# Kernel optimization log

Measured on AMD Instinct MI355X. Metric: run time of the kernel, lower is better.

## Reference

```python
import jax, jax.numpy as jnp
import numpy as np

TAU = 0.1
B = 4        # number of batches
S = 256      # spatial extent per axis
K = 128      # max peaks per batch (original caps total at num_batches*128)
NEG = -jnp.inf


def _l2norm(x, eps=1e-12):
    n = jnp.sqrt(jnp.sum(x * x, axis=1, keepdims=True))
    return x / jnp.maximum(n, eps)


def _peak_pool(coords, feats, conf, mask):
    # Submanifold 3x3x3 sparse max-pool on conf and avg-pool on feats,
    # restricted to voxels with conf > tau (the original builds the spconv
    # tensors only from masked voxels). Neighbor lookup via sorted key hash.
    N = coords.shape[0]
    bidx = coords[:, 0]
    x, y, z = coords[:, 1], coords[:, 2], coords[:, 3]
    key = ((bidx * S + x) * S + y) * S + z
    order = jnp.argsort(key)
    skey = key[order]
    hmax = jnp.full((N,), NEG, dtype=conf.dtype)
    fsum = jnp.zeros_like(feats)
    cnt = jnp.zeros((N,), dtype=feats.dtype)
    for dx in (-1, 0, 1):
        for dy in (-1, 0, 1):
            for dz in (-1, 0, 1):
                nx, ny, nz = x + dx, y + dy, z + dz
                valid = (nx >= 0) & (nx < S) & (ny >= 0) & (ny < S) & (nz >= 0) & (nz < S)
                nkey = ((bidx * S + nx) * S + ny) * S + nz
                pos = jnp.minimum(jnp.searchsorted(skey, nkey), N - 1)
                j = order[pos]
                hit = valid & (skey[pos] == nkey) & mask[j]
                hmax = jnp.maximum(hmax, jnp.where(hit, conf[j], NEG))
                fsum = fsum + jnp.where(hit[:, None], feats[j], 0.0)
                cnt = cnt + hit.astype(feats.dtype)
    favg = fsum / jnp.maximum(cnt, 1.0)[:, None]
    return hmax, favg


def setup_inputs() -> dict:
    key = jax.random.key(0)
    ks = jax.random.split(key, 6)
    N, L, D = 800000, 64, 32
    batch = jax.random.randint(ks[0], (N, 1), 0, B, dtype=jnp.int32)
    xyz = jax.random.randint(ks[1], (N, 3), 0, S, dtype=jnp.int32)
    coords = jnp.concatenate([batch, xyz], axis=1)
    voxel_feats = jax.random.normal(ks[2], (N, L), jnp.float32)
    centroid_scores = jax.random.uniform(ks[3], (N, 1), jnp.float32)
    W = jax.random.normal(ks[4], (L, D), jnp.float32) * 0.05
    b = jnp.zeros((D,), jnp.float32)
    background = jax.random.normal(ks[5], (D,), jnp.float32) * 0.02
    return {"coords": coords, "voxel_feats": voxel_feats,
            "centroid_scores": centroid_scores, "W": W, "b": b,
            "background": background}


def reference(coords, voxel_feats, centroid_scores, W, b, background):
    conf = centroid_scores[:, 0]
    mask = conf > TAU
    hmax, peak_feats = _peak_pool(coords, voxel_feats, conf, mask)
    # CenterNet-style NMS: a masked voxel is a peak if it equals its local max
    peak_mask = mask & (hmax == conf)
    voxel_desc = _l2norm(voxel_feats @ W + b)           # [N, D]
    bidx = coords[:, 0]
    peak_conf, blocks = [], []
    for bi in range(B):
        score = jnp.where(peak_mask & (bidx == bi), conf, NEG)
        vals, idx = jax.lax.top_k(score, K)             # fixed K peaks/batch
        valid = jnp.isfinite(vals)
        cdesc = _l2norm(peak_feats[idx] @ W + b)        # [K, D]
        cdesc = jnp.where(valid[:, None], cdesc, 0.0)
        # per-batch layout: background descriptor first, then centroids
        blocks.append(jnp.concatenate([background[None, :], cdesc], axis=0))
        peak_conf.append(jnp.where(valid, vals, 0.0))
    full_desc = jnp.concatenate(blocks, axis=0)         # [B*(K+1), D]
    return jnp.stack(peak_conf, axis=0), voxel_desc, full_desc
```

## Files before the change

kernel.cpp:

```cpp
#include <hip/hip_runtime.h>
#include <math.h>

#define S 256
#define NB 4
#define TAU 0.1f
#define KSEL 128
#define LOG_TAB 21
#define TAB_SZ (1u << LOG_TAB)
#define TAB_MASK (TAB_SZ - 1)
#define EMPTY64 0xFFFFFFFFFFFFFFFFull
#define BM_WORDS (1u << 21)
#define NBINS 8192
#define BIN_BASE 0x3D800
#define CAND_CAP 4096
#define CPAD 32

typedef unsigned long long u64;
typedef unsigned int u32;

__device__ __forceinline__ u32 hash_key(int key) {
    u32 h = (u32)key * 0x9E3779B1u;
    h ^= h >> 15;
    return h & TAB_MASK;
}

__device__ __forceinline__ int conf_bin(float conf) {
    int bin = (int)(__float_as_uint(conf) >> 12) - BIN_BASE;
    return bin < 0 ? 0 : (bin > NBINS - 1 ? NBINS - 1 : bin);
}

__device__ __forceinline__ int tab_lookup(const u64* __restrict__ tab, int key) {
    u32 slot = hash_key(key);
    for (;;) {
        u64 e = tab[slot];
        if ((u32)(e >> 32) == (u32)key) return (int)(u32)e;
        if (e == EMPTY64) return -1;
        slot = (slot + 1) & TAB_MASK;
    }
}

__device__ __forceinline__ void desc_row(const float* __restrict__ feats,
                                         const float* __restrict__ W,
                                         const float* __restrict__ bias,
                                         float* __restrict__ voxel_desc, int i, int N) {
    if (i >= N) return;
    const float4* row4 = (const float4*)(feats + (size_t)i * 64);
    float4 r[16];
    #pragma unroll
    for (int k = 0; k < 16; k++) r[k] = row4[k];
    asm volatile("" ::: "memory");
    float acc[32];
    #pragma unroll
    for (int d = 0; d < 32; d++) acc[d] = bias[d];
    #pragma unroll
    for (int k = 0; k < 16; k++) {
        float4 f = r[k];
        const float* Wb = W + k * 4 * 32;
        #pragma unroll
        for (int d = 0; d < 32; d++) {
            acc[d] = fmaf(f.x, Wb[d], acc[d]);
            acc[d] = fmaf(f.y, Wb[32 + d], acc[d]);
            acc[d] = fmaf(f.z, Wb[64 + d], acc[d]);
            acc[d] = fmaf(f.w, Wb[96 + d], acc[d]);
        }
    }
    float ss = 0.f;
    #pragma unroll
    for (int d = 0; d < 32; d++) ss += acc[d] * acc[d];
    float inv = 1.0f / fmaxf(sqrtf(ss), 1e-12f);
    float4* out4 = (float4*)(voxel_desc + (size_t)i * 32);
    #pragma unroll
    for (int q = 0; q < 8; q++) {
        float4 o;
        o.x = acc[q * 4 + 0] * inv; o.y = acc[q * 4 + 1] * inv;
        o.z = acc[q * 4 + 2] * inv; o.w = acc[q * 4 + 3] * inv;
        out4[q] = o;
    }
}

__device__ __forceinline__ void insert_pt(const int* __restrict__ coords,
                                          const float* __restrict__ scores,
                                          u64* __restrict__ tab, u32* __restrict__ bm,
                                          int i, int N) {
    if (i >= N) return;
    int4 c = ((const int4*)coords)[i];
    float conf = scores[i];
    int key = ((c.x * S + c.y) * S + c.z) * S + c.w;
    if (conf > TAU) atomicOr(&bm[(u32)key >> 5], 1u << (key & 31));
    u64 ins = ((u64)(u32)key << 32) | (u32)i;
    u32 slot = hash_key(key);
    for (;;) {
        u64 e = tab[slot];
        if ((u32)(e >> 32) == (u32)key) { atomicMin(&tab[slot], ins); return; }
        if (e == EMPTY64) {
            u64 prev = atomicCAS(&tab[slot], EMPTY64, ins);
            if (prev == EMPTY64) return;
            if ((u32)(prev >> 32) == (u32)key) { atomicMin(&tab[slot], ins); return; }
        }
        slot = (slot + 1) & TAB_MASK;
    }
}

__global__ __launch_bounds__(256, 4) void k_ins_desc(const int* __restrict__ coords,
        const float* __restrict__ scores, u64* __restrict__ tab, u32* __restrict__ bm,
        const float* __restrict__ feats, const float* __restrict__ W,
        const float* __restrict__ bias, float* __restrict__ voxel_desc,
        int N, int nIns, int nDesc, int descRow0) {
    int g = blockIdx.x / 3, r = blockIdx.x % 3;
    if (r < 2) {
        int ib = g * 2 + r;
        if (ib >= nIns) return;
        insert_pt(coords, scores, tab, bm, ib * 256 + threadIdx.x, N);
    } else {
        if (g >= nDesc) return;
        desc_row(feats, W, bias, voxel_desc, descRow0 + g * 256 + threadIdx.x, N);
    }
}

__device__ __forceinline__ void peak_block(const int* __restrict__ coords,
        const float* __restrict__ scores, const u64* __restrict__ tab,
        const u32* __restrict__ bm, u64* __restrict__ peaks, int* __restrict__ cnt,
        int* __restrict__ hist, int N, int pcap, int pb) {
    int i = pb * 256 + threadIdx.x;
    bool alive = (i < N);
    int ii = alive ? i : 0;
    int4 c = ((const int4*)coords)[ii];
    float conf = alive ? scores[ii] : -1.0f;
    int kb = ((c.x * S + c.y) * S + c.z) * S + c.w;
    bool ispeak = false;
    if (alive && conf > TAU) {
        u32 m27 = 0;
        u32 vzm = (u32)((c.w > 0) ? 1 : 0) | 2u | (u32)((c.w < S - 1) ? 4 : 0);
        #pragma unroll
        for (int dx = -1; dx <= 1; dx++) {
            if ((unsigned)(c.y + dx) >= S) continue;
            #pragma unroll
            for (int dy = -1; dy <= 1; dy++) {
                if ((unsigned)(c.z + dy) >= S) continue;
                int nk = kb + dx * (S * S) + dy * S;
                u32 idx = (u32)nk >> 5;
                int sft = nk & 31;
                u32 w0 = bm[idx];
                u32 b3;
                if (sft >= 1 && sft <= 30) {
                    b3 = (w0 >> (sft - 1)) & 7u;
                } else if (sft == 0) {
                    u32 wm = (nk >= 32) ? bm[idx - 1] : 0u;
                    b3 = ((wm >> 31) & 1u) | ((w0 & 3u) << 1);
                } else {
                    u32 wp = (idx + 1 < BM_WORDS) ? bm[idx + 1] : 0u;
                    b3 = ((w0 >> 30) & 3u) | ((wp & 1u) << 2);
                }
                b3 &= vzm;
                int p = ((dx + 1) * 3 + (dy + 1)) * 3;
                m27 |= b3 << p;
            }
        }
        float hmax = -INFINITY;
        while (m27) {
            int q = __builtin_ctz(m27);
            m27 &= m27 - 1;
            int dx = q / 9 - 1;
            int rr = q % 9;
            int dy = rr / 3 - 1, dz = rr % 3 - 1;
            int j = tab_lookup(tab, kb + dx * (S * S) + dy * S + dz);
            if (j >= 0) hmax = fmaxf(hmax, scores[j]);
        }
        ispeak = (hmax == conf);
    }

    if (ispeak) atomicAdd(&hist[c.x * NBINS + conf_bin(conf)], 1);

    __shared__ int wcnt[4][NB];
    __shared__ int bbase[NB];
    int w = threadIdx.x >> 6;
    int lane = threadIdx.x & 63;
    u64 lmask_lt = (lane == 63) ? 0x7FFFFFFFFFFFFFFFull : ((1ull << lane) - 1ull);
    u64 mb[NB];
    #pragma unroll
    for (int b = 0; b < NB; b++) {
        mb[b] = __ballot(ispeak && (c.x == b));
        if (lane == 0) wcnt[w][b] = __popcll(mb[b]);
    }
    __syncthreads();
    if (threadIdx.x < NB) {
        int b = threadIdx.x;
        int tot = wcnt[0][b] + wcnt[1][b] + wcnt[2][b] + wcnt[3][b];
        bbase[b] = tot > 0 ? atomicAdd(&cnt[b * CPAD], tot) : 0;
    }
    __syncthreads();
    if (ispeak) {
        int b = c.x;
        int pre = 0;
        for (int w2 = 0; w2 < w; w2++) pre += wcnt[w2][b];
        int rank = __popcll(mb[b] & lmask_lt);
        int pidx = bbase[b] + pre + rank;
        if (pidx < pcap)
            peaks[(size_t)b * pcap + pidx] =
                ((u64)__float_as_uint(conf) << 32) | (u32)(~(u32)i);
    }
}

__global__ __launch_bounds__(256, 4) void k_peak_desc(const int* __restrict__ coords,
        const float* __restrict__ scores, const u64* __restrict__ tab,
        const u32* __restrict__ bm, u64* __restrict__ peaks, int* __restrict__ cnt,
        int* __restrict__ hist, const float* __restrict__ feats,
        const float* __restrict__ W, const float* __restrict__ bias,
        float* __restrict__ voxel_desc, int N, int pcap,
        int nPeak, int nDesc, int descRow0) {
    int g = blockIdx.x / 3, r = blockIdx.x % 3;
    if (r < 2) {
        int pb = g * 2 + r;
        if (pb >= nPeak) return;
        peak_block(coords, scores, tab, bm, peaks, cnt, hist, N, pcap, pb);
    } else {
        if (g >= nDesc) return;
        desc_row(feats, W, bias, voxel_desc, descRow0 + g * 256 + threadIdx.x, N);
    }
}

__global__ void k_thresh(const int* __restrict__ hist, const int* __restrict__ cnt,
                         u32* __restrict__ thrbin, int pcap) {
    int w = threadIdx.x >> 6;
    int lane = threadIdx.x & 63;
    if (w >= NB) return;
    int n = cnt[w * CPAD]; if (n > pcap) n = pcap;
    int need = n < KSEL ? n : KSEL;
    const int* h = hist + w * NBINS;
    int running = 0;
    u32 thr = 0;
    for (int hi = NBINS - 64; hi >= 0; hi -= 64) {
        int v = h[hi + lane];
        int s = v;
        #pragma unroll
        for (int off = 1; off < 64; off <<= 1) {
            int o = __shfl_down(s, off);
            if (lane + off < 64) s += o;
        }
        int csum = __shfl(s, 0);
        if (running + csum >= need) {
            u64 m = __ballot(running + s >= need);
            int top = 63 - __builtin_clzll(m);
            thr = (u32)(hi + top);
            break;
        }
        running += csum;
    }
    if (lane == 0) thrbin[w] = thr;
}

__global__ void k_compact(const u64* __restrict__ peaks, const int* __restrict__ cnt,
                          const u32* __restrict__ thrbin, u64* __restrict__ cand,
                          int* __restrict__ ccnt, int pcap) {
    int t = blockIdx.x * blockDim.x + threadIdx.x;
    int b = t / pcap;
    if (b >= NB) return;
    int e = t % pcap;
    int n = cnt[b * CPAD]; if (n > pcap) n = pcap;
    if (e >= n) return;
    u64 key = peaks[(size_t)b * pcap + e];
    float conf = __uint_as_float((u32)(key >> 32));
    if (conf_bin(conf) >= (int)thrbin[b]) {
        int p = atomicAdd(&ccnt[b * CPAD], 1);
        if (p < CAND_CAP) cand[(size_t)b * CAND_CAP + p] = key;
    }
}

__global__ void k_topk(u64* __restrict__ cand, const int* __restrict__ ccnt,
                       u64* __restrict__ bufA, u64* __restrict__ selected) {
    int b = blockIdx.x;
    int tid = threadIdx.x;
    __shared__ int hist[256];
    __shared__ int sh_split, sh_above, sh_selc, sh_candc;
    u64* sel = selected + b * KSEL;
    u64* pcur = cand + (size_t)b * CAND_CAP;
    u64* pnxt = bufA + (size_t)b * CAND_CAP;
    int n = ccnt[b * CPAD];
    if (n > CAND_CAP) n = CAND_CAP;
    int need = KSEL, nsel = 0;

    for (int byte = 7; byte >= 0; byte--) {
        if (need <= 0) break;
        if (n <= need) {
            for (int idx = tid; idx < n; idx += blockDim.x) sel[nsel + idx] = pcur[idx];
            nsel += n; need -= n; n = 0;
            break;
        }
        hist[tid] = 0;
        __syncthreads();
        int shift = byte * 8;
        for (int idx = tid; idx < n; idx += blockDim.x)
            atomicAdd(&hist[(int)((pcur[idx] >> shift) & 255)], 1);
        __syncthreads();
        if (tid == 0) {
            int above = 0, s = 255;
            for (; s > 0; s--) {
                if (above + hist[s] >= need) break;
                above += hist[s];
            }
            sh_split = s; sh_above = above; sh_selc = 0; sh_candc = 0;
        }
        __syncthreads();
        int s = sh_split;
        for (int idx = tid; idx < n; idx += blockDim.x) {
            u64 e = pcur[idx];
            int bv = (int)((e >> shift) & 255);
            if (bv > s) { int p = atomicAdd(&sh_selc, 1); sel[nsel + p] = e; }
            else if (bv == s) { int p = atomicAdd(&sh_candc, 1); pnxt[p] = e; }
        }
        __syncthreads();
        nsel += sh_above; need -= sh_above; n = sh_candc;
        u64* t = pcur; pcur = pnxt; pnxt = t;
        __syncthreads();
    }
    if (need > 0 && n > 0) {
        int take = need < n ? need : n;
        for (int idx = tid; idx < take; idx += blockDim.x) sel[nsel + idx] = pcur[idx];
        nsel += take;
    }
    for (int idx = nsel + tid; idx < KSEL; idx += blockDim.x) sel[idx] = 0;
    __syncthreads();

    __shared__ u64 sk[KSEL];
    if (tid < KSEL) sk[tid] = sel[tid];
    __syncthreads();
    for (int k = 2; k <= KSEL; k <<= 1) {
        for (int j = k >> 1; j > 0; j >>= 1) {
            if (tid < KSEL) {
                int ixj = tid ^ j;
                if (ixj > tid) {
                    u64 a = sk[tid], c2 = sk[ixj];
                    bool upper = (tid & k) != 0;
                    if (upper ? (a > c2) : (a < c2)) { sk[tid] = c2; sk[ixj] = a; }
                }
            }
            __syncthreads();
        }
    }
    if (tid < KSEL) sel[tid] = sk[tid];
}

__global__ void k_final(const int* __restrict__ coords, const float* __restrict__ feats,
                        const float* __restrict__ scores, const float* __restrict__ W,
                        const float* __restrict__ bias, const float* __restrict__ background,
                        const u64* __restrict__ tab, const u64* __restrict__ selected,
                        float* __restrict__ out, int N) {
    int gw = (blockIdx.x * blockDim.x + threadIdx.x) >> 6;
    int lane = threadIdx.x & 63;
    float* full = out + NB * KSEL + (size_t)N * 32;
    if (gw >= NB * KSEL) {
        int b = gw - NB * KSEL;
        if (b < NB && lane < 32)
            full[(size_t)(b * (KSEL + 1)) * 32 + lane] = background[lane];
        return;
    }
    int b = gw >> 7, k = gw & 127;
    u64 key = selected[gw];
    float* row = full + (size_t)(b * (KSEL + 1) + 1 + k) * 32;
    if (key == 0ull) {
        if (lane == 0) out[gw] = 0.f;
        if (lane < 32) row[lane] = 0.f;
        return;
    }
    float conf = __uint_as_float((u32)(key >> 32));
    int i = (int)(~(u32)key);
    if (lane == 0) out[gw] = conf;
    int4 c = ((const int4*)coords)[i];
    int kb = ((c.x * S + c.y) * S + c.z) * S + c.w;
    int j = -1; bool hit = false;
    if (lane < 27) {
        int dx = lane / 9 - 1, r = lane % 9;
        int dy = r / 3 - 1, dz = r % 3 - 1;
        int nx = c.y + dx, ny = c.z + dy, nz = c.w + dz;
        if ((unsigned)nx < S && (unsigned)ny < S && (unsigned)nz < S) {
            j = tab_lookup(tab, kb + dx * (S * S) + dy * S + dz);
            if (j >= 0) hit = scores[j] > TAU;
        }
    }
    u64 hm = __ballot(hit);
    int c27 = __popcll(hm);
    float fsum = 0.f;
    u64 m = hm;
    while (m) {
        int src = __ffsll((long long)m) - 1;
        m &= m - 1;
        int jj = __shfl(j, src);
        fsum += feats[(size_t)jj * 64 + lane];
    }
    float favg = fsum / fmaxf((float)c27, 1.0f);
    int d = lane & 31;
    float acc = bias[d];
    #pragma unroll
    for (int l = 0; l < 64; l++) {
        float fl = __shfl(favg, l);
        acc = fmaf(fl, W[l * 32 + d], acc);
    }
    float ss = acc * acc;
    #pragma unroll
    for (int off = 1; off < 32; off <<= 1) ss += __shfl_xor(ss, off);
    float inv = 1.0f / fmaxf(sqrtf(ss), 1e-12f);
    if (lane < 32) row[lane] = acc * inv;
}

extern "C" void kernel_launch(void* const* d_in, const int* in_sizes, int n_in,
                              void* d_out, int out_size, void* d_ws, size_t ws_size,
                              hipStream_t stream) {
    const int* coords = (const int*)d_in[0];
    const float* feats = (const float*)d_in[1];
    const float* scores = (const float*)d_in[2];
    const float* W = (const float*)d_in[3];
    const float* bias = (const float*)d_in[4];
    const float* background = (const float*)d_in[5];
    int N = in_sizes[0] / 4;
    float* out = (float*)d_out;
    int pcap = N / 2;

    char* ws = (char*)d_ws;
    size_t off = 0;
    u64* tab = (u64*)(ws + off); off += (size_t)TAB_SZ * 8;
    size_t zoff = off;
    u32* bm = (u32*)(ws + off); off += (size_t)BM_WORDS * 4;
    int* hist = (int*)(ws + off); off += (size_t)NB * NBINS * 4;
    int* cnt = (int*)(ws + off); off += (size_t)NB * CPAD * 4;
    int* ccnt = (int*)(ws + off); off += (size_t)NB * CPAD * 4;
    u32* thrbin = (u32*)(ws + off); off += 256;
    size_t zlen = off - zoff;
    u64* peaks = (u64*)(ws + off); off += (size_t)NB * pcap * 8;
    u64* cand = (u64*)(ws + off); off += (size_t)NB * CAND_CAP * 8;
    u64* bufA = (u64*)(ws + off); off += (size_t)NB * CAND_CAP * 8;
    u64* selected = (u64*)(ws + off); off += (size_t)NB * KSEL * 8;

    int nBlk = (N + 255) / 256;
    int nDescA = nBlk / 2;
    int rowsA = nDescA * 256;
    int nDescB = (N - rowsA + 255) / 256;
    int grid1 = 3 * ((nBlk + 1) / 2 > nDescA ? (nBlk + 1) / 2 : nDescA);
    int grid2 = 3 * ((nBlk + 1) / 2 > nDescB ? (nBlk + 1) / 2 : nDescB);

    hipMemsetAsync(tab, 0xFF, (size_t)TAB_SZ * 8, stream);
    hipMemsetAsync(ws + zoff, 0, zlen, stream);
    k_ins_desc<<<grid1, 256, 0, stream>>>(coords, scores, tab, bm,
                                          feats, W, bias, out + NB * KSEL,
                                          N, nBlk, nDescA, 0);
    k_peak_desc<<<grid2, 256, 0, stream>>>(coords, scores, tab, bm, peaks, cnt, hist,
                                           feats, W, bias, out + NB * KSEL,
                                           N, pcap, nBlk, nDescB, rowsA);
    k_thresh<<<1, 256, 0, stream>>>(hist, cnt, thrbin, pcap);
    k_compact<<<(NB * pcap + 255) / 256, 256, 0, stream>>>(peaks, cnt, thrbin, cand, ccnt, pcap);
    k_topk<<<NB, 256, 0, stream>>>(cand, ccnt, bufA, selected);
    k_final<<<(NB * KSEL + NB + 3) / 4, 256, 0, stream>>>(coords, feats, scores, W, bias,
                                                          background, tab, selected, out, N);
}
```

Baseline: 281.1 us.

## Add coarse 2x occupancy bitmap to skip empty neighbor rows in peak test

Builds a second, coarse bitmap at half resolution during insertion and uses it in the peak test to skip fine-bitmap row reads for neighbor xy columns with no masked voxels. The center voxel's score is taken from a direct lookup rather than the bitmap loop. It also shifts the descriptor row split between the two fused kernels toward the second kernel and replaces the compiler memory fence with a scheduling barrier. This adds extra atomics at insert time and a larger memset in exchange for fewer scattered bitmap loads.

```diff
diff --git a/kernel.cpp b/kernel.cpp
--- a/kernel.cpp
+++ b/kernel.cpp
@@ -10,6 +10,7 @@
 #define TAB_MASK (TAB_SZ - 1)
 #define EMPTY64 0xFFFFFFFFFFFFFFFFull
 #define BM_WORDS (1u << 21)
+#define CBM_WORDS (1u << 18)
 #define NBINS 8192
 #define BIN_BASE 0x3D800
 #define CAND_CAP 4096
@@ -48,7 +49,7 @@
     float4 r[16];
     #pragma unroll
     for (int k = 0; k < 16; k++) r[k] = row4[k];
-    asm volatile("" ::: "memory");
+    __builtin_amdgcn_sched_barrier(0);
     float acc[32];
     #pragma unroll
     for (int d = 0; d < 32; d++) acc[d] = bias[d];
@@ -81,12 +82,16 @@
 __device__ __forceinline__ void insert_pt(const int* __restrict__ coords,
                                           const float* __restrict__ scores,
                                           u64* __restrict__ tab, u32* __restrict__ bm,
-                                          int i, int N) {
+                                          u32* __restrict__ cbm, int i, int N) {
     if (i >= N) return;
     int4 c = ((const int4*)coords)[i];
     float conf = scores[i];
     int key = ((c.x * S + c.y) * S + c.z) * S + c.w;
-    if (conf > TAU) atomicOr(&bm[(u32)key >> 5], 1u << (key & 31));
+    if (conf > TAU) {
+        atomicOr(&bm[(u32)key >> 5], 1u << (key & 31));
+        int ck = ((c.x * 128 + (c.y >> 1)) * 128 + (c.z >> 1)) * 128 + (c.w >> 1);
+        atomicOr(&cbm[(u32)ck >> 5], 1u << (ck & 31));
+    }
     u64 ins = ((u64)(u32)key << 32) | (u32)i;
     u32 slot = hash_key(key);
     for (;;) {
@@ -103,14 +108,14 @@
 
 __global__ __launch_bounds__(256, 4) void k_ins_desc(const int* __restrict__ coords,
         const float* __restrict__ scores, u64* __restrict__ tab, u32* __restrict__ bm,
-        const float* __restrict__ feats, const float* __restrict__ W,
-        const float* __restrict__ bias, float* __restrict__ voxel_desc,
-        int N, int nIns, int nDesc, int descRow0) {
+        u32* __restrict__ cbm, const float* __restrict__ feats,
+        const float* __restrict__ W, const float* __restrict__ bias,
+        float* __restrict__ voxel_desc, int N, int nIns, int nDesc, int descRow0) {
     int g = blockIdx.x / 3, r = blockIdx.x % 3;
     if (r < 2) {
         int ib = g * 2 + r;
         if (ib >= nIns) return;
-        insert_pt(coords, scores, tab, bm, ib * 256 + threadIdx.x, N);
+        insert_pt(coords, scores, tab, bm, cbm, ib * 256 + threadIdx.x, N);
     } else {
         if (g >= nDesc) return;
         desc_row(feats, W, bias, voxel_desc, descRow0 + g * 256 + threadIdx.x, N);
@@ -119,7 +124,8 @@
 
 __device__ __forceinline__ void peak_block(const int* __restrict__ coords,
         const float* __restrict__ scores, const u64* __restrict__ tab,
-        const u32* __restrict__ bm, u64* __restrict__ peaks, int* __restrict__ cnt,
+        const u32* __restrict__ bm, const u32* __restrict__ cbm,
+        u64* __restrict__ peaks, int* __restrict__ cnt,
         int* __restrict__ hist, int N, int pcap, int pb) {
     int i = pb * 256 + threadIdx.x;
     bool alive = (i < N);
@@ -129,14 +135,37 @@
     int kb = ((c.x * S + c.y) * S + c.z) * S + c.w;
     bool ispeak = false;
     if (alive && conf > TAU) {
+        int cxl = (c.y > 0) ? ((c.y - 1) >> 1) : 0;
+        int cyl = (c.z > 0) ? ((c.z - 1) >> 1) : 0;
+        int czl = (c.w > 0) ? ((c.w - 1) >> 1) : 0;
+        int czh = (c.w < S - 1) ? ((c.w + 1) >> 1) : 127;
+        int nzb = czh - czl + 1;
+        u32 zmask = (nzb == 2) ? 3u : 1u;
+        bool czor[2][2];
+        #pragma unroll
+        for (int ix = 0; ix < 2; ix++) {
+            int ccx = cxl + ix; if (ccx > 127) ccx = 127;
+            #pragma unroll
+            for (int iy = 0; iy < 2; iy++) {
+                int ccy = cyl + iy; if (ccy > 127) ccy = 127;
+                int base = ((c.x * 128 + ccx) * 128 + ccy) * 128 + czl;
+                u32 wv = cbm[(u32)base >> 5];
+                int sh = base & 31;
+                u32 bits = wv >> sh;
+                if (sh == 31 && nzb == 2) bits |= (cbm[((u32)base >> 5) + 1] & 1u) << 1;
+                czor[ix][iy] = (bits & zmask) != 0;
+            }
+        }
         u32 m27 = 0;
         u32 vzm = (u32)((c.w > 0) ? 1 : 0) | 2u | (u32)((c.w < S - 1) ? 4 : 0);
         #pragma unroll
         for (int dx = -1; dx <= 1; dx++) {
             if ((unsigned)(c.y + dx) >= S) continue;
+            int ix = ((c.y + dx) >> 1) - cxl;
             #pragma unroll
             for (int dy = -1; dy <= 1; dy++) {
                 if ((unsigned)(c.z + dy) >= S) continue;
+                if (!czor[ix][((c.z + dy) >> 1) - cyl]) continue;
                 int nk = kb + dx * (S * S) + dy * S;
                 u32 idx = (u32)nk >> 5;
                 int sft = nk & 31;
@@ -156,7 +185,9 @@
                 m27 |= b3 << p;
             }
         }
-        float hmax = -INFINITY;
+        int j0 = tab_lookup(tab, kb);
+        float hmax = (j0 == i) ? conf : scores[j0];
+        m27 &= ~(1u << 13);
         while (m27) {
             int q = __builtin_ctz(m27);
             m27 &= m27 - 1;
@@ -203,7 +234,8 @@
 
 __global__ __launch_bounds__(256, 4) void k_peak_desc(const int* __restrict__ coords,
         const float* __restrict__ scores, const u64* __restrict__ tab,
-        const u32* __restrict__ bm, u64* __restrict__ peaks, int* __restrict__ cnt,
+        const u32* __restrict__ bm, const u32* __restrict__ cbm,
+        u64* __restrict__ peaks, int* __restrict__ cnt,
         int* __restrict__ hist, const float* __restrict__ feats,
         const float* __restrict__ W, const float* __restrict__ bias,
         float* __restrict__ voxel_desc, int N, int pcap,
@@ -212,7 +244,7 @@
     if (r < 2) {
         int pb = g * 2 + r;
         if (pb >= nPeak) return;
-        peak_block(coords, scores, tab, bm, peaks, cnt, hist, N, pcap, pb);
+        peak_block(coords, scores, tab, bm, cbm, peaks, cnt, hist, N, pcap, pb);
     } else {
         if (g >= nDesc) return;
         desc_row(feats, W, bias, voxel_desc, descRow0 + g * 256 + threadIdx.x, N);
@@ -420,6 +452,7 @@
     u64* tab = (u64*)(ws + off); off += (size_t)TAB_SZ * 8;
     size_t zoff = off;
     u32* bm = (u32*)(ws + off); off += (size_t)BM_WORDS * 4;
+    u32* cbm = (u32*)(ws + off); off += (size_t)CBM_WORDS * 4;
     int* hist = (int*)(ws + off); off += (size_t)NB * NBINS * 4;
     int* cnt = (int*)(ws + off); off += (size_t)NB * CPAD * 4;
     int* ccnt = (int*)(ws + off); off += (size_t)NB * CPAD * 4;
@@ -431,20 +464,21 @@
     u64* selected = (u64*)(ws + off); off += (size_t)NB * KSEL * 8;
 
     int nBlk = (N + 255) / 256;
-    int nDescA = nBlk / 2;
+    int nDescA = (int)(((long)nBlk * 45) / 100);
     int rowsA = nDescA * 256;
     int nDescB = (N - rowsA + 255) / 256;
-    int grid1 = 3 * ((nBlk + 1) / 2 > nDescA ? (nBlk + 1) / 2 : nDescA);
-    int grid2 = 3 * ((nBlk + 1) / 2 > nDescB ? (nBlk + 1) / 2 : nDescB);
+    int half = (nBlk + 1) / 2;
+    int g1 = half > nDescA ? half : nDescA;
+    int g2 = half > nDescB ? half : nDescB;
 
     hipMemsetAsync(tab, 0xFF, (size_t)TAB_SZ * 8, stream);
     hipMemsetAsync(ws + zoff, 0, zlen, stream);
-    k_ins_desc<<<grid1, 256, 0, stream>>>(coords, scores, tab, bm,
-                                          feats, W, bias, out + NB * KSEL,
-                                          N, nBlk, nDescA, 0);
-    k_peak_desc<<<grid2, 256, 0, stream>>>(coords, scores, tab, bm, peaks, cnt, hist,
+    k_ins_desc<<<3 * g1, 256, 0, stream>>>(coords, scores, tab, bm, cbm,
                                            feats, W, bias, out + NB * KSEL,
-                                           N, pcap, nBlk, nDescB, rowsA);
+                                           N, nBlk, nDescA, 0);
+    k_peak_desc<<<3 * g2, 256, 0, stream>>>(coords, scores, tab, bm, cbm, peaks, cnt, hist,
+                                            feats, W, bias, out + NB * KSEL,
+                                            N, pcap, nBlk, nDescB, rowsA);
     k_thresh<<<1, 256, 0, stream>>>(hist, cnt, thrbin, pcap);
     k_compact<<<(NB * pcap + 255) / 256, 256, 0, stream>>>(peaks, cnt, thrbin, cand, ccnt, pcap);
     k_topk<<<NB, 256, 0, stream>>>(cand, ccnt, bufA, selected);
```

Measured after the change: 299.5 us. 1.07x slower.
